# Kernel tuning notes

Hardware: AMD Instinct MI355X
Metric: run time of the kernel (lower is better)

Reference implementation:

```python
import jax, jax.numpy as jnp
import numpy as np

BETA = 0.5
ITEM_NUM = 100000
REGION_NUM = 1000
EMBED = 128
HIDDEN = 256
B, H = 1024, 256


def setup_inputs() -> dict:
    key = jax.random.key(0)
    ks = jax.random.split(key, 10)
    history = jax.random.randint(ks[0], (B, H), 0, ITEM_NUM)
    target = jax.random.randint(ks[1], (B,), 0, ITEM_NUM)
    history_region = jax.random.randint(ks[2], (B, H), 0, REGION_NUM)
    target_region = jax.random.randint(ks[3], (B,), 0, REGION_NUM)
    E_hist = 0.01 * jax.random.normal(ks[4], (ITEM_NUM, EMBED), dtype=jnp.float32)
    E_targ = 0.01 * jax.random.normal(ks[5], (ITEM_NUM, EMBED), dtype=jnp.float32)
    E_reg = 0.01 * jax.random.normal(ks[6], (REGION_NUM, EMBED), dtype=jnp.float32)
    lim1 = 1.0 / np.sqrt(2 * EMBED)
    W1 = jax.random.uniform(ks[7], (2 * EMBED, HIDDEN), jnp.float32, -lim1, lim1)
    b1 = jnp.zeros((HIDDEN,), jnp.float32)
    lim2 = 1.0 / np.sqrt(HIDDEN)
    w2 = jax.random.uniform(ks[8], (HIDDEN,), jnp.float32, -lim2, lim2)
    return {"history": history, "target": target,
            "history_region": history_region, "target_region": target_region,
            "E_hist": E_hist, "E_targ": E_targ, "E_reg": E_reg,
            "W1": W1, "b1": b1, "w2": w2}


def reference(history, target, history_region, target_region,
              E_hist, E_targ, E_reg, W1, b1, w2):
    # gathers + concat: hist [B,H,2d], tgt [B,2d]
    hist = jnp.concatenate([E_hist[history], E_reg[history_region]], axis=-1)
    tgt = jnp.concatenate([E_targ[target], E_reg[target_region]], axis=-1)
    # elementwise product broadcast over history dim
    inp = hist * tgt[:, None, :]                      # [B,H,2d]
    hid = jax.nn.relu(jnp.einsum('bhd,dk->bhk', inp, W1) + b1)
    scores = jnp.einsum('bhk,k->bh', hid, w2)         # [B,H]
    mask = (history != target[:, None]).astype(scores.dtype)
    exp_a = jnp.exp(scores) * mask                    # [B,H]
    denom = jnp.power(jnp.sum(exp_a, axis=-1), BETA)  # [B]
    attn = exp_a / denom[:, None]                     # [B,H]
    # weighted reduction: sum_h sum_d hist*attn*tgt
    pred = jnp.einsum('bhd,bh,bd->b', hist, attn, tgt)
    return jax.nn.sigmoid(pred)
```

## Files before the change

kernel.cpp:

```cpp
#include <hip/hip_runtime.h>
#include <hip/hip_bf16.h>

#define NB 1024
#define NH 256
#define EMB 128
#define TWOD 256
#define HID 256
#define ROWS 128
#define BPB 2
#define NBLK (NB * BPB)
#define HISTN 100000
#define REGN 1000

typedef __attribute__((ext_vector_type(4))) float f32x4;
typedef __attribute__((ext_vector_type(8))) short bf16x8;

__device__ __forceinline__ unsigned short f2bf(float f) {
  union { float f; unsigned u; } v; v.f = f;
  unsigned u = v.u;
  unsigned r = (u + 0x7fffu + ((u >> 16) & 1u)) >> 16;
  return (unsigned short)r;
}

__device__ __forceinline__ float bf2f(short s) {
  union { unsigned u; float f; } c;
  c.u = ((unsigned)(unsigned short)s) << 16;
  return c.f;
}

__device__ __forceinline__ bf16x8 pack8(f32x4 a, f32x4 b) {
  union { bf16x8 w; unsigned u[4]; } r;
  float2 p;
  union { __hip_bfloat162 h; unsigned u; } c;
  p.x = a[0]; p.y = a[1]; c.h = __float22bfloat162_rn(p); r.u[0] = c.u;
  p.x = a[2]; p.y = a[3]; c.h = __float22bfloat162_rn(p); r.u[1] = c.u;
  p.x = b[0]; p.y = b[1]; c.h = __float22bfloat162_rn(p); r.u[2] = c.u;
  p.x = b[2]; p.y = b[3]; c.h = __float22bfloat162_rn(p); r.u[3] = c.u;
  return r.w;
}

__global__ __launch_bounds__(256) void prep_w1t(const float* __restrict__ W1,
                                                unsigned short* __restrict__ W1T) {
  const int d = blockIdx.x;
  const int n = threadIdx.x;
  W1T[(size_t)n * TWOD + d] = f2bf(W1[(size_t)d * HID + n]);
}

__global__ __launch_bounds__(256) void prep_ebf(const float* __restrict__ Eh,
                                                const float* __restrict__ Er,
                                                unsigned short* __restrict__ EBH,
                                                unsigned short* __restrict__ EBR) {
  const long long NE_H = (long long)HISTN * EMB;
  const long long NE_R = (long long)REGN * EMB;
  long long i = ((long long)blockIdx.x * 256 + threadIdx.x) * 8;
  if (i >= NE_H + NE_R) return;
  const float* src; unsigned short* dst; long long off;
  if (i < NE_H) { src = Eh; dst = EBH; off = i; }
  else          { src = Er; dst = EBR; off = i - NE_H; }
  f32x4 v0 = *(const f32x4*)(src + off);
  f32x4 v1 = *(const f32x4*)(src + off + 4);
  *(bf16x8*)(dst + off) = pack8(v0, v1);
}

__global__ __launch_bounds__(512, 4) void nais_main(
    const int* __restrict__ history, const int* __restrict__ target,
    const int* __restrict__ hregion, const int* __restrict__ tregion,
    const float* __restrict__ E_targ, const float* __restrict__ E_reg,
    const unsigned short* __restrict__ EBH, const unsigned short* __restrict__ EBR,
    const unsigned short* __restrict__ W1T, const float* __restrict__ b1,
    const float* __restrict__ w2,
    float* __restrict__ part_se, float* __restrict__ part_sd)
{
  const int blk = blockIdx.x;
  const int b = blk >> 1;
  const int r0 = (blk & 1) * ROWS;
  const int tid = threadIdx.x;
  const int lane = tid & 63;
  const int wave = tid >> 6;
  const int l15 = lane & 15;
  const int lhi = lane >> 4;

  __shared__ __align__(16) unsigned short A_h[ROWS * EMB];
  __shared__ __align__(16) unsigned short A_r[ROWS * EMB];
  __shared__ __align__(16) float tgt_lds[TWOD];
  __shared__ int keys_h[ROWS];
  __shared__ int keys_r[ROWS];
  __shared__ float dot_lds[ROWS];
  __shared__ float score_parts[8][ROWS];

  const int tgt_item = target[b];

  if (tid < ROWS) {
    keys_h[tid] = history[b * NH + r0 + tid];
  } else if (tid < 2 * ROWS) {
    keys_r[tid - ROWS] = hregion[b * NH + r0 + (tid - ROWS)];
  } else {
    const int c = tid - 2 * ROWS;
    tgt_lds[c] = (c < EMB) ? E_targ[(size_t)target[b] * EMB + c]
                           : E_reg[(size_t)tregion[b] * EMB + (c - EMB)];
  }
  __syncthreads();

  {
    #pragma unroll
    for (int q = 0; q < 4; ++q) {
      const int quad = wave * 4 + q;
      const int r = quad * 4 + (lane >> 4);
      const int g = (lane & 15) ^ (r & 7);
      const int kh = keys_h[r];
      const unsigned short* gh = EBH + (size_t)kh * EMB + g * 8;
      __builtin_amdgcn_global_load_lds(
          (const __attribute__((address_space(1))) void*)gh,
          (__attribute__((address_space(3))) void*)&A_h[quad * 4 * EMB],
          16, 0, 0);
      const int kr = keys_r[r];
      const unsigned short* gr = EBR + (size_t)kr * EMB + g * 8;
      __builtin_amdgcn_global_load_lds(
          (const __attribute__((address_space(1))) void*)gr,
          (__attribute__((address_space(3))) void*)&A_r[quad * 4 * EMB],
          16, 0, 0);
    }
  }
  asm volatile("s_waitcnt vmcnt(0)" ::: "memory");
  __syncthreads();

  {
    const int row = wave * 16 + (lane >> 2);
    const int seg = lane & 3;
    unsigned short* panel = (seg < 2) ? A_h : A_r;
    const int g0 = (seg & 1) * 8;
    float dsum = 0.f;
    #pragma unroll
    for (int j = 0; j < 8; ++j) {
      const int g = (g0 + j) ^ (row & 7);
      bf16x8* ap = (bf16x8*)&panel[row * EMB + g * 8];
      bf16x8 a = *ap;
      const int kg = seg * 64 + j * 8;
      f32x4 t0 = *(const f32x4*)&tgt_lds[kg];
      f32x4 t1 = *(const f32x4*)&tgt_lds[kg + 4];
      f32x4 lo, hi;
      #pragma unroll
      for (int e = 0; e < 4; ++e) { lo[e] = bf2f(a[e]); hi[e] = bf2f(a[4 + e]); }
      lo *= t0; hi *= t1;
      dsum += lo[0] + lo[1] + lo[2] + lo[3] + hi[0] + hi[1] + hi[2] + hi[3];
      *ap = pack8(lo, hi);
    }
    dsum += __shfl_xor(dsum, 1);
    dsum += __shfl_xor(dsum, 2);
    if (seg == 0) dot_lds[row] = dsum;
  }
  __syncthreads();

  {
    const int col0 = wave * 32;
    float b1v[2], w2v[2];
    #pragma unroll
    for (int n = 0; n < 2; ++n) {
      const int colh = col0 + n * 16 + l15;
      b1v[n] = b1[colh];
      w2v[n] = w2[colh];
    }

    f32x4 acc[2][4][2];
    #pragma unroll
    for (int c = 0; c < 2; ++c)
      #pragma unroll
      for (int m = 0; m < 4; ++m)
        #pragma unroll
        for (int n = 0; n < 2; ++n)
          acc[c][m][n] = (f32x4){0.f, 0.f, 0.f, 0.f};

    #pragma unroll
    for (int kk = 0; kk < 8; ++kk) {
      const unsigned short* panel = (kk < 4) ? A_h : A_r;
      bf16x8 bfr[2];
      #pragma unroll
      for (int n = 0; n < 2; ++n) {
        const int colh = col0 + n * 16 + l15;
        bfr[n] = *(const bf16x8*)(W1T + (size_t)colh * TWOD + kk * 32 + lhi * 8);
      }
      bf16x8 af[2][4];
      #pragma unroll
      for (int c = 0; c < 2; ++c)
        #pragma unroll
        for (int m = 0; m < 4; ++m) {
          const int row = c * 64 + m * 16 + l15;
          const int gk = ((kk & 3) * 4 + lhi) ^ (row & 7);
          af[c][m] = *(const bf16x8*)&panel[row * EMB + gk * 8];
        }
      __builtin_amdgcn_s_setprio(1);
      #pragma unroll
      for (int c = 0; c < 2; ++c)
        #pragma unroll
        for (int m = 0; m < 4; ++m)
          #pragma unroll
          for (int n = 0; n < 2; ++n)
            acc[c][m][n] = __builtin_amdgcn_mfma_f32_16x16x32_bf16(af[c][m], bfr[n], acc[c][m][n], 0, 0, 0);
      __builtin_amdgcn_s_setprio(0);
    }

    #pragma unroll
    for (int c = 0; c < 2; ++c) {
      #pragma unroll
      for (int m = 0; m < 4; ++m) {
        #pragma unroll
        for (int r = 0; r < 4; ++r) {
          float p = 0.f;
          #pragma unroll
          for (int n = 0; n < 2; ++n) {
            float hv = acc[c][m][n][r] + b1v[n];
            hv = hv > 0.f ? hv : 0.f;
            p += hv * w2v[n];
          }
          p += __shfl_xor(p, 1);
          p += __shfl_xor(p, 2);
          p += __shfl_xor(p, 4);
          p += __shfl_xor(p, 8);
          if (l15 == 0) score_parts[wave][c * 64 + m * 16 + lhi * 4 + r] = p;
        }
      }
    }
  }
  __syncthreads();

  if (wave < 2) {
    const int lrow = wave * 64 + lane;
    float sc = 0.f;
    #pragma unroll
    for (int w = 0; w < 8; ++w) sc += score_parts[w][lrow];
    float e = (keys_h[lrow] != tgt_item) ? expf(sc) : 0.f;
    float ed = e * dot_lds[lrow];
    #pragma unroll
    for (int off = 32; off >= 1; off >>= 1) {
      e += __shfl_xor(e, off);
      ed += __shfl_xor(ed, off);
    }
    if (lane == 0) {
      part_se[blk * 2 + wave] = e;
      part_sd[blk * 2 + wave] = ed;
    }
  }
}

__global__ __launch_bounds__(256) void finalize(const float* __restrict__ part_se,
                                                const float* __restrict__ part_sd,
                                                float* __restrict__ out) {
  const int b = blockIdx.x * 256 + threadIdx.x;
  if (b < NB) {
    float se = 0.f, sd = 0.f;
    #pragma unroll
    for (int i = 0; i < BPB * 2; ++i) {
      se += part_se[b * BPB * 2 + i];
      sd += part_sd[b * BPB * 2 + i];
    }
    const float pred = (se > 0.f) ? (sd / sqrtf(se)) : 0.f;
    out[b] = 1.f / (1.f + expf(-pred));
  }
}

extern "C" void kernel_launch(void* const* d_in, const int* in_sizes, int n_in,
                              void* d_out, int out_size, void* d_ws, size_t ws_size,
                              hipStream_t stream) {
  const int* history = (const int*)d_in[0];
  const int* target  = (const int*)d_in[1];
  const int* hregion = (const int*)d_in[2];
  const int* tregion = (const int*)d_in[3];
  const float* E_hist = (const float*)d_in[4];
  const float* E_targ = (const float*)d_in[5];
  const float* E_reg  = (const float*)d_in[6];
  const float* W1 = (const float*)d_in[7];
  const float* b1 = (const float*)d_in[8];
  const float* w2 = (const float*)d_in[9];
  float* out = (float*)d_out;

  char* p = (char*)d_ws;
  unsigned short* W1T = (unsigned short*)p;  p += (size_t)TWOD * HID * 2;
  unsigned short* EBR = (unsigned short*)p;  p += (size_t)REGN * EMB * 2;
  float* part_se = (float*)p;                p += (size_t)NBLK * 2 * 4;
  float* part_sd = (float*)p;                p += (size_t)NBLK * 2 * 4;
  unsigned short* EBH = (unsigned short*)p;

  prep_w1t<<<TWOD, HID, 0, stream>>>(W1, W1T);
  {
    const long long tot8 = ((long long)HISTN * EMB + (long long)REGN * EMB) / 8;
    const int blocks = (int)((tot8 + 255) / 256);
    prep_ebf<<<blocks, 256, 0, stream>>>(E_hist, E_reg, EBH, EBR);
  }
  nais_main<<<NBLK, 512, 0, stream>>>(history, target, hregion, tregion,
                                      E_targ, E_reg, EBH, EBR, W1T, b1, w2,
                                      part_se, part_sd);
  finalize<<<(NB + 255) / 256, 256, 0, stream>>>(part_se, part_sd, out);
}
```

Measured before the change: 94.50 us.

## Pipeline history chunks with double-buffered gather DMA and fuse finalize into main kernel

The main kernel now runs one block per batch row and walks the 256 history rows in four 64-row chunks. The gather DMA for the next chunk goes into a second LDS buffer and overlaps the MFMA work on the current chunk. The exp/dot accumulation and the final sigmoid move into the main kernel, which removes the finalize launch and the partial-sum buffers. The two prep kernels are merged into a single launch. In exchange, the grid is half as large, there are more barriers per block, and the per-chunk work is smaller.

After: 97.45 us. 3.1% more time.

```diff
diff --git a/kernel.cpp b/kernel.cpp
--- a/kernel.cpp
+++ b/kernel.cpp
@@ -6,9 +6,8 @@
 #define EMB 128
 #define TWOD 256
 #define HID 256
-#define ROWS 128
-#define BPB 2
-#define NBLK (NB * BPB)
+#define CROWS 64
+#define NCH 4
 #define HISTN 100000
 #define REGN 1000
 
@@ -39,27 +38,30 @@
   return r.w;
 }
 
-__global__ __launch_bounds__(256) void prep_w1t(const float* __restrict__ W1,
-                                                unsigned short* __restrict__ W1T) {
-  const int d = blockIdx.x;
-  const int n = threadIdx.x;
-  W1T[(size_t)n * TWOD + d] = f2bf(W1[(size_t)d * HID + n]);
-}
-
-__global__ __launch_bounds__(256) void prep_ebf(const float* __restrict__ Eh,
-                                                const float* __restrict__ Er,
-                                                unsigned short* __restrict__ EBH,
-                                                unsigned short* __restrict__ EBR) {
-  const long long NE_H = (long long)HISTN * EMB;
-  const long long NE_R = (long long)REGN * EMB;
-  long long i = ((long long)blockIdx.x * 256 + threadIdx.x) * 8;
-  if (i >= NE_H + NE_R) return;
-  const float* src; unsigned short* dst; long long off;
-  if (i < NE_H) { src = Eh; dst = EBH; off = i; }
-  else          { src = Er; dst = EBR; off = i - NE_H; }
-  f32x4 v0 = *(const f32x4*)(src + off);
-  f32x4 v1 = *(const f32x4*)(src + off + 4);
-  *(bf16x8*)(dst + off) = pack8(v0, v1);
+#define NE_H ((long long)HISTN * EMB)
+#define NE_R ((long long)REGN * EMB)
+#define EBF_BLOCKS ((int)((NE_H + NE_R + 2047) / 2048))
+#define PREP_BLOCKS (EBF_BLOCKS + TWOD)
+
+__global__ __launch_bounds__(256) void prep_all(
+    const float* __restrict__ W1, const float* __restrict__ Eh,
+    const float* __restrict__ Er, unsigned short* __restrict__ W1T,
+    unsigned short* __restrict__ EBH, unsigned short* __restrict__ EBR) {
+  const int blk = blockIdx.x;
+  if (blk < EBF_BLOCKS) {
+    long long i = ((long long)blk * 256 + threadIdx.x) * 8;
+    if (i >= NE_H + NE_R) return;
+    const float* src; unsigned short* dst; long long off;
+    if (i < NE_H) { src = Eh; dst = EBH; off = i; }
+    else          { src = Er; dst = EBR; off = i - NE_H; }
+    f32x4 v0 = *(const f32x4*)(src + off);
+    f32x4 v1 = *(const f32x4*)(src + off + 4);
+    *(bf16x8*)(dst + off) = pack8(v0, v1);
+  } else {
+    const int d = blk - EBF_BLOCKS;
+    const int n = threadIdx.x;
+    W1T[(size_t)n * TWOD + d] = f2bf(W1[(size_t)d * HID + n]);
+  }
 }
 
 __global__ __launch_bounds__(512, 4) void nais_main(
@@ -68,76 +70,70 @@
     const float* __restrict__ E_targ, const float* __restrict__ E_reg,
     const unsigned short* __restrict__ EBH, const unsigned short* __restrict__ EBR,
     const unsigned short* __restrict__ W1T, const float* __restrict__ b1,
-    const float* __restrict__ w2,
-    float* __restrict__ part_se, float* __restrict__ part_sd)
+    const float* __restrict__ w2, float* __restrict__ out)
 {
-  const int blk = blockIdx.x;
-  const int b = blk >> 1;
-  const int r0 = (blk & 1) * ROWS;
+  const int b = blockIdx.x;
   const int tid = threadIdx.x;
   const int lane = tid & 63;
   const int wave = tid >> 6;
   const int l15 = lane & 15;
   const int lhi = lane >> 4;
 
-  __shared__ __align__(16) unsigned short A_h[ROWS * EMB];
-  __shared__ __align__(16) unsigned short A_r[ROWS * EMB];
+  __shared__ __align__(16) unsigned short A_h[2][CROWS * EMB];
+  __shared__ __align__(16) unsigned short A_r[2][CROWS * EMB];
   __shared__ __align__(16) float tgt_lds[TWOD];
-  __shared__ int keys_h[ROWS];
-  __shared__ int keys_r[ROWS];
-  __shared__ float dot_lds[ROWS];
-  __shared__ float score_parts[8][ROWS];
+  __shared__ int keys_h[NH];
+  __shared__ int keys_r[NH];
+  __shared__ float dot_lds[2][CROWS];
+  __shared__ float score_parts[8][CROWS];
 
   const int tgt_item = target[b];
 
-  if (tid < ROWS) {
-    keys_h[tid] = history[b * NH + r0 + tid];
-  } else if (tid < 2 * ROWS) {
-    keys_r[tid - ROWS] = hregion[b * NH + r0 + (tid - ROWS)];
+  if (tid < NH) {
+    keys_h[tid] = history[b * NH + tid];
+    tgt_lds[tid] = (tid < EMB) ? E_targ[(size_t)target[b] * EMB + tid]
+                               : E_reg[(size_t)tregion[b] * EMB + (tid - EMB)];
   } else {
-    const int c = tid - 2 * ROWS;
-    tgt_lds[c] = (c < EMB) ? E_targ[(size_t)target[b] * EMB + c]
-                           : E_reg[(size_t)tregion[b] * EMB + (c - EMB)];
+    keys_r[tid - NH] = hregion[b * NH + (tid - NH)];
   }
   __syncthreads();
 
-  {
-    #pragma unroll
-    for (int q = 0; q < 4; ++q) {
-      const int quad = wave * 4 + q;
-      const int r = quad * 4 + (lane >> 4);
-      const int g = (lane & 15) ^ (r & 7);
-      const int kh = keys_h[r];
-      const unsigned short* gh = EBH + (size_t)kh * EMB + g * 8;
+  const int dma_r4 = lane >> 4;
+  auto DMA_CHUNK = [&](int chunk, int bufsel) {
+    #pragma unroll
+    for (int q = 0; q < 2; ++q) {
+      const int rl = q * 4 + dma_r4;
+      const int prow = wave * 8 + rl;
+      const int g = (lane & 15) ^ rl;
+      const unsigned short* gh = EBH + (size_t)keys_h[chunk * CROWS + prow] * EMB + g * 8;
       __builtin_amdgcn_global_load_lds(
           (const __attribute__((address_space(1))) void*)gh,
-          (__attribute__((address_space(3))) void*)&A_h[quad * 4 * EMB],
+          (__attribute__((address_space(3))) void*)&A_h[bufsel][(wave * 8 + q * 4) * EMB],
           16, 0, 0);
-      const int kr = keys_r[r];
-      const unsigned short* gr = EBR + (size_t)kr * EMB + g * 8;
+      const unsigned short* gr = EBR + (size_t)keys_r[chunk * CROWS + prow] * EMB + g * 8;
       __builtin_amdgcn_global_load_lds(
           (const __attribute__((address_space(1))) void*)gr,
-          (__attribute__((address_space(3))) void*)&A_r[quad * 4 * EMB],
+          (__attribute__((address_space(3))) void*)&A_r[bufsel][(wave * 8 + q * 4) * EMB],
           16, 0, 0);
     }
-  }
-  asm volatile("s_waitcnt vmcnt(0)" ::: "memory");
-  __syncthreads();
-
-  {
-    const int row = wave * 16 + (lane >> 2);
-    const int seg = lane & 3;
-    unsigned short* panel = (seg < 2) ? A_h : A_r;
-    const int g0 = (seg & 1) * 8;
+  };
+
+  const int f_rl = lane & 7;
+  const int f_seg = lane >> 3;
+  const int f_pan = f_seg & 1;
+  const int f_gb = (f_seg >> 1) * 4;
+  auto FOLD_CHUNK = [&](int bufsel) {
+    const int prow = wave * 8 + f_rl;
+    unsigned short* panel = f_pan ? &A_r[bufsel][0] : &A_h[bufsel][0];
     float dsum = 0.f;
     #pragma unroll
-    for (int j = 0; j < 8; ++j) {
-      const int g = (g0 + j) ^ (row & 7);
-      bf16x8* ap = (bf16x8*)&panel[row * EMB + g * 8];
+    for (int j = 0; j < 4; ++j) {
+      const int q = f_gb + j;
+      const int gl = q ^ f_rl;
+      bf16x8* ap = (bf16x8*)&panel[prow * EMB + gl * 8];
       bf16x8 a = *ap;
-      const int kg = seg * 64 + j * 8;
-      f32x4 t0 = *(const f32x4*)&tgt_lds[kg];
-      f32x4 t1 = *(const f32x4*)&tgt_lds[kg + 4];
+      const f32x4 t0 = *(const f32x4*)&tgt_lds[f_pan * EMB + q * 8];
+      const f32x4 t1 = *(const f32x4*)&tgt_lds[f_pan * EMB + q * 8 + 4];
       f32x4 lo, hi;
       #pragma unroll
       for (int e = 0; e < 4; ++e) { lo[e] = bf2f(a[e]); hi[e] = bf2f(a[4 + e]); }
@@ -145,116 +141,116 @@
       dsum += lo[0] + lo[1] + lo[2] + lo[3] + hi[0] + hi[1] + hi[2] + hi[3];
       *ap = pack8(lo, hi);
     }
-    dsum += __shfl_xor(dsum, 1);
-    dsum += __shfl_xor(dsum, 2);
-    if (seg == 0) dot_lds[row] = dsum;
-  }
+    dsum += __shfl_xor(dsum, 8);
+    dsum += __shfl_xor(dsum, 16);
+    dsum += __shfl_xor(dsum, 32);
+    if (f_seg == 0) dot_lds[bufsel][prow] = dsum;
+  };
+
+  const int col0 = wave * 32;
+  float b1v[2], w2v[2];
+  #pragma unroll
+  for (int n = 0; n < 2; ++n) {
+    b1v[n] = b1[col0 + n * 16 + l15];
+    w2v[n] = w2[col0 + n * 16 + l15];
+  }
+
+  DMA_CHUNK(0, 0);
+  asm volatile("s_waitcnt vmcnt(0)" ::: "memory");
+  __builtin_amdgcn_sched_barrier(0);
+  FOLD_CHUNK(0);
   __syncthreads();
 
-  {
-    const int col0 = wave * 32;
-    float b1v[2], w2v[2];
-    #pragma unroll
-    for (int n = 0; n < 2; ++n) {
-      const int colh = col0 + n * 16 + l15;
-      b1v[n] = b1[colh];
-      w2v[n] = w2[colh];
-    }
-
-    f32x4 acc[2][4][2];
-    #pragma unroll
-    for (int c = 0; c < 2; ++c)
+  float acc_e = 0.f, acc_ed = 0.f;
+
+  #pragma unroll
+  for (int t = 0; t < NCH; ++t) {
+    const int buf = t & 1;
+
+    f32x4 acc[4][2];
+    #pragma unroll
+    for (int m = 0; m < 4; ++m)
+      #pragma unroll
+      for (int n = 0; n < 2; ++n)
+        acc[m][n] = (f32x4){0.f, 0.f, 0.f, 0.f};
+
+    #pragma unroll
+    for (int kk = 0; kk < 8; ++kk) {
+      const unsigned short* panel = (kk < 4) ? &A_h[buf][0] : &A_r[buf][0];
+      bf16x8 bfr[2];
+      #pragma unroll
+      for (int n = 0; n < 2; ++n)
+        bfr[n] = *(const bf16x8*)(W1T + (size_t)(col0 + n * 16 + l15) * TWOD + kk * 32 + lhi * 8);
+      bf16x8 af[4];
+      #pragma unroll
+      for (int m = 0; m < 4; ++m) {
+        const int row = m * 16 + l15;
+        const int gk = ((kk & 3) * 4 + lhi) ^ (row & 7);
+        af[m] = *(const bf16x8*)&panel[row * EMB + gk * 8];
+      }
+      __builtin_amdgcn_s_setprio(1);
       #pragma unroll
       for (int m = 0; m < 4; ++m)
         #pragma unroll
         for (int n = 0; n < 2; ++n)
-          acc[c][m][n] = (f32x4){0.f, 0.f, 0.f, 0.f};
-
-    #pragma unroll
-    for (int kk = 0; kk < 8; ++kk) {
-      const unsigned short* panel = (kk < 4) ? A_h : A_r;
-      bf16x8 bfr[2];
-      #pragma unroll
-      for (int n = 0; n < 2; ++n) {
-        const int colh = col0 + n * 16 + l15;
-        bfr[n] = *(const bf16x8*)(W1T + (size_t)colh * TWOD + kk * 32 + lhi * 8);
+          acc[m][n] = __builtin_amdgcn_mfma_f32_16x16x32_bf16(af[m], bfr[n], acc[m][n], 0, 0, 0);
+      __builtin_amdgcn_s_setprio(0);
+    }
+
+    if (t < NCH - 1) {
+      __builtin_amdgcn_sched_barrier(0);
+      DMA_CHUNK(t + 1, buf ^ 1);
+      __builtin_amdgcn_sched_barrier(0);
+    }
+
+    #pragma unroll
+    for (int m = 0; m < 4; ++m) {
+      #pragma unroll
+      for (int r = 0; r < 4; ++r) {
+        float p = 0.f;
+        #pragma unroll
+        for (int n = 0; n < 2; ++n) {
+          float hv = acc[m][n][r] + b1v[n];
+          hv = hv > 0.f ? hv : 0.f;
+          p += hv * w2v[n];
+        }
+        p += __shfl_xor(p, 1);
+        p += __shfl_xor(p, 2);
+        p += __shfl_xor(p, 4);
+        p += __shfl_xor(p, 8);
+        if (l15 == 0) score_parts[wave][m * 16 + lhi * 4 + r] = p;
       }
-      bf16x8 af[2][4];
-      #pragma unroll
-      for (int c = 0; c < 2; ++c)
-        #pragma unroll
-        for (int m = 0; m < 4; ++m) {
-          const int row = c * 64 + m * 16 + l15;
-          const int gk = ((kk & 3) * 4 + lhi) ^ (row & 7);
-          af[c][m] = *(const bf16x8*)&panel[row * EMB + gk * 8];
-        }
-      __builtin_amdgcn_s_setprio(1);
-      #pragma unroll
-      for (int c = 0; c < 2; ++c)
-        #pragma unroll
-        for (int m = 0; m < 4; ++m)
-          #pragma unroll
-          for (int n = 0; n < 2; ++n)
-            acc[c][m][n] = __builtin_amdgcn_mfma_f32_16x16x32_bf16(af[c][m], bfr[n], acc[c][m][n], 0, 0, 0);
-      __builtin_amdgcn_s_setprio(0);
-    }
-
-    #pragma unroll
-    for (int c = 0; c < 2; ++c) {
-      #pragma unroll
-      for (int m = 0; m < 4; ++m) {
-        #pragma unroll
-        for (int r = 0; r < 4; ++r) {
-          float p = 0.f;
-          #pragma unroll
-          for (int n = 0; n < 2; ++n) {
-            float hv = acc[c][m][n][r] + b1v[n];
-            hv = hv > 0.f ? hv : 0.f;
-            p += hv * w2v[n];
-          }
-          p += __shfl_xor(p, 1);
-          p += __shfl_xor(p, 2);
-          p += __shfl_xor(p, 4);
-          p += __shfl_xor(p, 8);
-          if (l15 == 0) score_parts[wave][c * 64 + m * 16 + lhi * 4 + r] = p;
-        }
-      }
-    }
-  }
-  __syncthreads();
-
-  if (wave < 2) {
-    const int lrow = wave * 64 + lane;
-    float sc = 0.f;
-    #pragma unroll
-    for (int w = 0; w < 8; ++w) sc += score_parts[w][lrow];
-    float e = (keys_h[lrow] != tgt_item) ? expf(sc) : 0.f;
-    float ed = e * dot_lds[lrow];
+    }
+    __syncthreads();
+
+    if (t < NCH - 1) {
+      asm volatile("s_waitcnt vmcnt(0)" ::: "memory");
+      __builtin_amdgcn_sched_barrier(0);
+      FOLD_CHUNK(buf ^ 1);
+    }
+
+    if (wave == 0) {
+      float sc = 0.f;
+      #pragma unroll
+      for (int w = 0; w < 8; ++w) sc += score_parts[w][lane];
+      const float e = (keys_h[t * CROWS + lane] != tgt_item) ? expf(sc) : 0.f;
+      acc_e += e;
+      acc_ed += e * dot_lds[buf][lane];
+    }
+    if (t < NCH - 1) __syncthreads();
+  }
+
+  if (wave == 0) {
+    float se = acc_e, sd = acc_ed;
     #pragma unroll
     for (int off = 32; off >= 1; off >>= 1) {
-      e += __shfl_xor(e, off);
-      ed += __shfl_xor(ed, off);
+      se += __shfl_xor(se, off);
+      sd += __shfl_xor(sd, off);
     }
     if (lane == 0) {
-      part_se[blk * 2 + wave] = e;
-      part_sd[blk * 2 + wave] = ed;
-    }
-  }
-}
-
-__global__ __launch_bounds__(256) void finalize(const float* __restrict__ part_se,
-                                                const float* __restrict__ part_sd,
-                                                float* __restrict__ out) {
-  const int b = blockIdx.x * 256 + threadIdx.x;
-  if (b < NB) {
-    float se = 0.f, sd = 0.f;
-    #pragma unroll
-    for (int i = 0; i < BPB * 2; ++i) {
-      se += part_se[b * BPB * 2 + i];
-      sd += part_sd[b * BPB * 2 + i];
-    }
-    const float pred = (se > 0.f) ? (sd / sqrtf(se)) : 0.f;
-    out[b] = 1.f / (1.f + expf(-pred));
+      const float pred = (se > 0.f) ? (sd / sqrtf(se)) : 0.f;
+      out[b] = 1.f / (1.f + expf(-pred));
+    }
   }
 }
 
@@ -276,18 +272,9 @@
   char* p = (char*)d_ws;
   unsigned short* W1T = (unsigned short*)p;  p += (size_t)TWOD * HID * 2;
   unsigned short* EBR = (unsigned short*)p;  p += (size_t)REGN * EMB * 2;
-  float* part_se = (float*)p;                p += (size_t)NBLK * 2 * 4;
-  float* part_sd = (float*)p;                p += (size_t)NBLK * 2 * 4;
   unsigned short* EBH = (unsigned short*)p;
 
-  prep_w1t<<<TWOD, HID, 0, stream>>>(W1, W1T);
-  {
-    const long long tot8 = ((long long)HISTN * EMB + (long long)REGN * EMB) / 8;
-    const int blocks = (int)((tot8 + 255) / 256);
-    prep_ebf<<<blocks, 256, 0, stream>>>(E_hist, E_reg, EBH, EBR);
-  }
-  nais_main<<<NBLK, 512, 0, stream>>>(history, target, hregion, tregion,
-                                      E_targ, E_reg, EBH, EBR, W1T, b1, w2,
-                                      part_se, part_sd);
-  finalize<<<(NB + 255) / 256, 256, 0, stream>>>(part_se, part_sd, out);
-}
+  prep_all<<<PREP_BLOCKS, 256, 0, stream>>>(W1, E_hist, E_reg, W1T, EBH, EBR);
+  nais_main<<<NB, 512, 0, stream>>>(history, target, hregion, tregion,
+                                    E_targ, E_reg, EBH, EBR, W1T, b1, w2, out);
+}
```

## Fold target into W1 fragments, gather fp32 rows directly, compute dots via MFMA

Applied to the files above, without the earlier changes.

Removes the whole-table bf16 conversion pre-pass and instead gathers fp32 embedding rows straight from E_hist/E_reg, converting them to bf16 while writing them into LDS. The elementwise product with the target is moved algebraically into the per-block W1 fragments, which are scaled by the target vector and held in registers, so the separate LDS multiply pass and one barrier go away. The hist·tgt dot products are computed by extra MFMAs on wave 0. Occupancy hint drops from 4 to 2 blocks because of higher register use. Gathering fp32 rows doubles the bytes per gathered row, but the conversion pass over the full 100k-row table is no longer needed.

Result: slower. 130.8 us (+38.5%).

```diff
diff --git a/kernel.cpp b/kernel.cpp
--- a/kernel.cpp
+++ b/kernel.cpp
@@ -9,8 +9,6 @@
 #define ROWS 128
 #define BPB 2
 #define NBLK (NB * BPB)
-#define HISTN 100000
-#define REGN 1000
 
 typedef __attribute__((ext_vector_type(4))) float f32x4;
 typedef __attribute__((ext_vector_type(8))) short bf16x8;
@@ -46,27 +44,11 @@
   W1T[(size_t)n * TWOD + d] = f2bf(W1[(size_t)d * HID + n]);
 }
 
-__global__ __launch_bounds__(256) void prep_ebf(const float* __restrict__ Eh,
-                                                const float* __restrict__ Er,
-                                                unsigned short* __restrict__ EBH,
-                                                unsigned short* __restrict__ EBR) {
-  const long long NE_H = (long long)HISTN * EMB;
-  const long long NE_R = (long long)REGN * EMB;
-  long long i = ((long long)blockIdx.x * 256 + threadIdx.x) * 8;
-  if (i >= NE_H + NE_R) return;
-  const float* src; unsigned short* dst; long long off;
-  if (i < NE_H) { src = Eh; dst = EBH; off = i; }
-  else          { src = Er; dst = EBR; off = i - NE_H; }
-  f32x4 v0 = *(const f32x4*)(src + off);
-  f32x4 v1 = *(const f32x4*)(src + off + 4);
-  *(bf16x8*)(dst + off) = pack8(v0, v1);
-}
-
-__global__ __launch_bounds__(512, 4) void nais_main(
+__global__ __launch_bounds__(512, 2) void nais_main(
     const int* __restrict__ history, const int* __restrict__ target,
     const int* __restrict__ hregion, const int* __restrict__ tregion,
-    const float* __restrict__ E_targ, const float* __restrict__ E_reg,
-    const unsigned short* __restrict__ EBH, const unsigned short* __restrict__ EBR,
+    const float* __restrict__ E_hist, const float* __restrict__ E_targ,
+    const float* __restrict__ E_reg,
     const unsigned short* __restrict__ W1T, const float* __restrict__ b1,
     const float* __restrict__ w2,
     float* __restrict__ part_se, float* __restrict__ part_sd)
@@ -79,10 +61,13 @@
   const int wave = tid >> 6;
   const int l15 = lane & 15;
   const int lhi = lane >> 4;
+  const int l31 = lane & 31;
+  const int halfsel = lane >> 5;
 
   __shared__ __align__(16) unsigned short A_h[ROWS * EMB];
   __shared__ __align__(16) unsigned short A_r[ROWS * EMB];
   __shared__ __align__(16) float tgt_lds[TWOD];
+  __shared__ __align__(16) unsigned short tgtbf[TWOD];
   __shared__ int keys_h[ROWS];
   __shared__ int keys_r[ROWS];
   __shared__ float dot_lds[ROWS];
@@ -96,128 +81,141 @@
     keys_r[tid - ROWS] = hregion[b * NH + r0 + (tid - ROWS)];
   } else {
     const int c = tid - 2 * ROWS;
-    tgt_lds[c] = (c < EMB) ? E_targ[(size_t)target[b] * EMB + c]
-                           : E_reg[(size_t)tregion[b] * EMB + (c - EMB)];
+    const float v = (c < EMB) ? E_targ[(size_t)target[b] * EMB + c]
+                              : E_reg[(size_t)tregion[b] * EMB + (c - EMB)];
+    tgt_lds[c] = v;
+    tgtbf[c] = f2bf(v);
   }
   __syncthreads();
 
   {
-    #pragma unroll
-    for (int q = 0; q < 4; ++q) {
-      const int quad = wave * 4 + q;
-      const int r = quad * 4 + (lane >> 4);
-      const int g = (lane & 15) ^ (r & 7);
-      const int kh = keys_h[r];
-      const unsigned short* gh = EBH + (size_t)kh * EMB + g * 8;
-      __builtin_amdgcn_global_load_lds(
-          (const __attribute__((address_space(1))) void*)gh,
-          (__attribute__((address_space(3))) void*)&A_h[quad * 4 * EMB],
-          16, 0, 0);
-      const int kr = keys_r[r];
-      const unsigned short* gr = EBR + (size_t)kr * EMB + g * 8;
-      __builtin_amdgcn_global_load_lds(
-          (const __attribute__((address_space(1))) void*)gr,
-          (__attribute__((address_space(3))) void*)&A_r[quad * 4 * EMB],
-          16, 0, 0);
-    }
-  }
-  asm volatile("s_waitcnt vmcnt(0)" ::: "memory");
+    const float* table = halfsel ? E_reg : E_hist;
+    const int* keys = halfsel ? keys_r : keys_h;
+    unsigned short* panel = halfsel ? A_r : A_h;
+    #pragma unroll
+    for (int pass = 0; pass < 2; ++pass) {
+      int key[8];
+      #pragma unroll
+      for (int s = 0; s < 8; ++s)
+        key[s] = keys[wave * 16 + pass * 8 + s];
+      f32x4 vb[8];
+      #pragma unroll
+      for (int s = 0; s < 8; ++s)
+        vb[s] = *(const f32x4*)(table + (size_t)key[s] * EMB + l31 * 4);
+      #pragma unroll
+      for (int s = 0; s < 8; ++s) {
+        const int row = wave * 16 + pass * 8 + s;
+        float2 f01; f01.x = vb[s][0]; f01.y = vb[s][1];
+        float2 f23; f23.x = vb[s][2]; f23.y = vb[s][3];
+        union { __hip_bfloat162 h; unsigned u; } c0, c1;
+        c0.h = __float22bfloat162_rn(f01);
+        c1.h = __float22bfloat162_rn(f23);
+        const int g = l31 >> 1;
+        const int gs = g ^ (row & 7);
+        unsigned* dst = (unsigned*)&panel[row * EMB + gs * 8] + (l31 & 1) * 2;
+        dst[0] = c0.u; dst[1] = c1.u;
+      }
+    }
+  }
+
+  const int col0 = wave * 32;
+  bf16x8 bfr[8][2];
+  #pragma unroll
+  for (int kk = 0; kk < 8; ++kk) {
+    const f32x4 t0 = *(const f32x4*)&tgt_lds[kk * 32 + lhi * 8];
+    const f32x4 t1 = *(const f32x4*)&tgt_lds[kk * 32 + lhi * 8 + 4];
+    #pragma unroll
+    for (int n = 0; n < 2; ++n) {
+      const bf16x8 w = *(const bf16x8*)(W1T + (size_t)(col0 + n * 16 + l15) * TWOD + kk * 32 + lhi * 8);
+      f32x4 lo, hi;
+      #pragma unroll
+      for (int e = 0; e < 4; ++e) {
+        lo[e] = bf2f(w[e]) * t0[e];
+        hi[e] = bf2f(w[4 + e]) * t1[e];
+      }
+      bfr[kk][n] = pack8(lo, hi);
+      asm volatile("" : "+a"(bfr[kk][n]));
+    }
+  }
+  float b1v[2], w2v[2];
+  #pragma unroll
+  for (int n = 0; n < 2; ++n) {
+    b1v[n] = b1[col0 + n * 16 + l15];
+    w2v[n] = w2[col0 + n * 16 + l15];
+  }
   __syncthreads();
 
-  {
-    const int row = wave * 16 + (lane >> 2);
-    const int seg = lane & 3;
-    unsigned short* panel = (seg < 2) ? A_h : A_r;
-    const int g0 = (seg & 1) * 8;
-    float dsum = 0.f;
-    #pragma unroll
-    for (int j = 0; j < 8; ++j) {
-      const int g = (g0 + j) ^ (row & 7);
-      bf16x8* ap = (bf16x8*)&panel[row * EMB + g * 8];
-      bf16x8 a = *ap;
-      const int kg = seg * 64 + j * 8;
-      f32x4 t0 = *(const f32x4*)&tgt_lds[kg];
-      f32x4 t1 = *(const f32x4*)&tgt_lds[kg + 4];
-      f32x4 lo, hi;
-      #pragma unroll
-      for (int e = 0; e < 4; ++e) { lo[e] = bf2f(a[e]); hi[e] = bf2f(a[4 + e]); }
-      lo *= t0; hi *= t1;
-      dsum += lo[0] + lo[1] + lo[2] + lo[3] + hi[0] + hi[1] + hi[2] + hi[3];
-      *ap = pack8(lo, hi);
-    }
-    dsum += __shfl_xor(dsum, 1);
-    dsum += __shfl_xor(dsum, 2);
-    if (seg == 0) dot_lds[row] = dsum;
-  }
-  __syncthreads();
-
-  {
-    const int col0 = wave * 32;
-    float b1v[2], w2v[2];
-    #pragma unroll
-    for (int n = 0; n < 2; ++n) {
-      const int colh = col0 + n * 16 + l15;
-      b1v[n] = b1[colh];
-      w2v[n] = w2[colh];
-    }
-
-    f32x4 acc[2][4][2];
+  f32x4 acc[2][4][2];
+  f32x4 acc2[2][4];
+  #pragma unroll
+  for (int c = 0; c < 2; ++c)
+    #pragma unroll
+    for (int m = 0; m < 4; ++m) {
+      acc2[c][m] = (f32x4){0.f, 0.f, 0.f, 0.f};
+      #pragma unroll
+      for (int n = 0; n < 2; ++n)
+        acc[c][m][n] = (f32x4){0.f, 0.f, 0.f, 0.f};
+    }
+
+  #pragma unroll
+  for (int kk = 0; kk < 8; ++kk) {
+    const unsigned short* panel = (kk < 4) ? A_h : A_r;
+    bf16x8 af[2][4];
     #pragma unroll
     for (int c = 0; c < 2; ++c)
       #pragma unroll
+      for (int m = 0; m < 4; ++m) {
+        const int row = c * 64 + m * 16 + l15;
+        const int gk = ((kk & 3) * 4 + lhi) ^ (row & 7);
+        af[c][m] = *(const bf16x8*)&panel[row * EMB + gk * 8];
+      }
+    __builtin_amdgcn_s_setprio(1);
+    #pragma unroll
+    for (int c = 0; c < 2; ++c)
+      #pragma unroll
       for (int m = 0; m < 4; ++m)
         #pragma unroll
         for (int n = 0; n < 2; ++n)
-          acc[c][m][n] = (f32x4){0.f, 0.f, 0.f, 0.f};
-
-    #pragma unroll
-    for (int kk = 0; kk < 8; ++kk) {
-      const unsigned short* panel = (kk < 4) ? A_h : A_r;
-      bf16x8 bfr[2];
-      #pragma unroll
-      for (int n = 0; n < 2; ++n) {
-        const int colh = col0 + n * 16 + l15;
-        bfr[n] = *(const bf16x8*)(W1T + (size_t)colh * TWOD + kk * 32 + lhi * 8);
-      }
-      bf16x8 af[2][4];
+          acc[c][m][n] = __builtin_amdgcn_mfma_f32_16x16x32_bf16(af[c][m], bfr[kk][n], acc[c][m][n], 0, 0, 0);
+    __builtin_amdgcn_s_setprio(0);
+    if (wave == 0) {
+      const bf16x8 tfr = *(const bf16x8*)&tgtbf[kk * 32 + lhi * 8];
       #pragma unroll
       for (int c = 0; c < 2; ++c)
         #pragma unroll
-        for (int m = 0; m < 4; ++m) {
-          const int row = c * 64 + m * 16 + l15;
-          const int gk = ((kk & 3) * 4 + lhi) ^ (row & 7);
-          af[c][m] = *(const bf16x8*)&panel[row * EMB + gk * 8];
+        for (int m = 0; m < 4; ++m)
+          acc2[c][m] = __builtin_amdgcn_mfma_f32_16x16x32_bf16(af[c][m], tfr, acc2[c][m], 0, 0, 0);
+    }
+  }
+
+  if (wave == 0 && l15 == 0) {
+    #pragma unroll
+    for (int c = 0; c < 2; ++c)
+      #pragma unroll
+      for (int m = 0; m < 4; ++m)
+        #pragma unroll
+        for (int r = 0; r < 4; ++r)
+          dot_lds[c * 64 + m * 16 + lhi * 4 + r] = acc2[c][m][r];
+  }
+
+  #pragma unroll
+  for (int c = 0; c < 2; ++c) {
+    #pragma unroll
+    for (int m = 0; m < 4; ++m) {
+      #pragma unroll
+      for (int r = 0; r < 4; ++r) {
+        float p = 0.f;
+        #pragma unroll
+        for (int n = 0; n < 2; ++n) {
+          float hv = acc[c][m][n][r] + b1v[n];
+          hv = hv > 0.f ? hv : 0.f;
+          p += hv * w2v[n];
         }
-      __builtin_amdgcn_s_setprio(1);
-      #pragma unroll
-      for (int c = 0; c < 2; ++c)
-        #pragma unroll
-        for (int m = 0; m < 4; ++m)
-          #pragma unroll
-          for (int n = 0; n < 2; ++n)
-            acc[c][m][n] = __builtin_amdgcn_mfma_f32_16x16x32_bf16(af[c][m], bfr[n], acc[c][m][n], 0, 0, 0);
-      __builtin_amdgcn_s_setprio(0);
-    }
-
-    #pragma unroll
-    for (int c = 0; c < 2; ++c) {
-      #pragma unroll
-      for (int m = 0; m < 4; ++m) {
-        #pragma unroll
-        for (int r = 0; r < 4; ++r) {
-          float p = 0.f;
-          #pragma unroll
-          for (int n = 0; n < 2; ++n) {
-            float hv = acc[c][m][n][r] + b1v[n];
-            hv = hv > 0.f ? hv : 0.f;
-            p += hv * w2v[n];
-          }
-          p += __shfl_xor(p, 1);
-          p += __shfl_xor(p, 2);
-          p += __shfl_xor(p, 4);
-          p += __shfl_xor(p, 8);
-          if (l15 == 0) score_parts[wave][c * 64 + m * 16 + lhi * 4 + r] = p;
-        }
+        p += __shfl_xor(p, 1);
+        p += __shfl_xor(p, 2);
+        p += __shfl_xor(p, 4);
+        p += __shfl_xor(p, 8);
+        if (l15 == 0) score_parts[wave][c * 64 + m * 16 + lhi * 4 + r] = p;
       }
     }
   }
@@ -275,19 +273,12 @@
 
   char* p = (char*)d_ws;
   unsigned short* W1T = (unsigned short*)p;  p += (size_t)TWOD * HID * 2;
-  unsigned short* EBR = (unsigned short*)p;  p += (size_t)REGN * EMB * 2;
   float* part_se = (float*)p;                p += (size_t)NBLK * 2 * 4;
-  float* part_sd = (float*)p;                p += (size_t)NBLK * 2 * 4;
-  unsigned short* EBH = (unsigned short*)p;
+  float* part_sd = (float*)p;
 
   prep_w1t<<<TWOD, HID, 0, stream>>>(W1, W1T);
-  {
-    const long long tot8 = ((long long)HISTN * EMB + (long long)REGN * EMB) / 8;
-    const int blocks = (int)((tot8 + 255) / 256);
-    prep_ebf<<<blocks, 256, 0, stream>>>(E_hist, E_reg, EBH, EBR);
-  }
   nais_main<<<NBLK, 512, 0, stream>>>(history, target, hregion, tregion,
-                                      E_targ, E_reg, EBH, EBR, W1T, b1, w2,
+                                      E_hist, E_targ, E_reg, W1T, b1, w2,
                                       part_se, part_sd);
   finalize<<<(NB + 255) / 256, 256, 0, stream>>>(part_se, part_sd, out);
 }
```
